# Kernel tuning notes

Hardware: AMD Instinct MI355X
Metric: run time of the kernel (lower is better)

The kernel has to match this reference:

```python
import jax, jax.numpy as jnp
import numpy as np

B, N, D_IN, D_OUT = 2, 4096, 768, 768


def setup_inputs() -> dict:
    key = jax.random.key(0)
    kx, kq, kk, kv = jax.random.split(key, 4)
    x = jax.random.normal(kx, (B, N, D_IN), dtype=jnp.float32)
    # Linear(d_in, d_out, bias=False) weights, stored as [d_in, d_out]
    scale = 1.0 / np.sqrt(D_IN)
    Wq = jax.random.normal(kq, (D_IN, D_OUT), dtype=jnp.float32) * scale
    Wk = jax.random.normal(kk, (D_IN, D_OUT), dtype=jnp.float32) * scale
    Wv = jax.random.normal(kv, (D_IN, D_OUT), dtype=jnp.float32) * scale
    return {"x": x, "Wq": Wq, "Wk": Wk, "Wv": Wv}


def reference(x, Wq, Wk, Wv):
    # q,k,v: [B, N, D_OUT]
    q = jnp.einsum('bnd,de->bne', x, Wq)
    k = jnp.einsum('bnd,de->bne', x, Wk)
    v = jnp.einsum('bnd,de->bne', x, Wv)
    # Full [B, N, N] score matrix (naive attention, as in source).
    # NOTE: source's masked_fill is non-in-place and discarded, so NO causal
    # mask is actually applied -- reproduced faithfully here.
    scores = jnp.einsum('bqe,bke->bqk', q, k) / jnp.sqrt(jnp.float32(k.shape[-1]))
    weights = jax.nn.softmax(scores, axis=-1)
    # dropout rate 0.0 / eval mode -> identity
    out = jnp.einsum('bqk,bke->bqe', weights, v)  # [B, N, D_OUT]
    return out
```

## Files before the change

kernel.cpp:

```cpp
#include <hip/hip_runtime.h>

typedef __bf16 bf16x8 __attribute__((ext_vector_type(8)));
typedef float f32x4 __attribute__((ext_vector_type(4)));

#define GAS __attribute__((address_space(1)))
#define LAS __attribute__((address_space(3)))

__device__ __forceinline__ unsigned short f32_to_bf16(float f) {
    unsigned int u = __float_as_uint(f);
    u += 0x7FFFu + ((u >> 16) & 1u);
    return (unsigned short)(u >> 16);
}

__device__ __forceinline__ void load16(const unsigned short* g, unsigned short* l) {
    __builtin_amdgcn_global_load_lds((GAS unsigned int*)g, (LAS unsigned int*)l, 16, 0, 0);
}

__global__ __launch_bounds__(256) void convert_f32_bf16(
    const float* __restrict__ in, unsigned short* __restrict__ out, int n4)
{
    int i = blockIdx.x * 256 + threadIdx.x;
    if (i < n4) {
        float4 v = ((const float4*)in)[i];
        ushort4 o;
        o.x = f32_to_bf16(v.x); o.y = f32_to_bf16(v.y);
        o.z = f32_to_bf16(v.z); o.w = f32_to_bf16(v.w);
        ((ushort4*)out)[i] = o;
    }
}

__global__ __launch_bounds__(1024) void transpose_w(
    const float* __restrict__ W0, const float* __restrict__ W1, const float* __restrict__ W2,
    unsigned short* __restrict__ T0, unsigned short* __restrict__ T1, unsigned short* __restrict__ T2)
{
    __shared__ float tile[32][33];
    const float* W = (blockIdx.z == 0) ? W0 : (blockIdx.z == 1) ? W1 : W2;
    unsigned short* T = (blockIdx.z == 0) ? T0 : (blockIdx.z == 1) ? T1 : T2;
    int r0 = blockIdx.y * 32, c0 = blockIdx.x * 32;
    tile[threadIdx.y][threadIdx.x] = W[(size_t)(r0 + threadIdx.y) * 768 + c0 + threadIdx.x];
    __syncthreads();
    T[(size_t)(c0 + threadIdx.y) * 768 + r0 + threadIdx.x] = f32_to_bf16(tile[threadIdx.x][threadIdx.y]);
}

template <typename CT>
__global__ __launch_bounds__(256) void gemm_nt(
    const unsigned short* __restrict__ A, const unsigned short* __restrict__ B,
    CT* __restrict__ C, int K, int lda, int ldb, int ldc,
    size_t sA, size_t sB, size_t sC, float alpha)
{
    A += (size_t)blockIdx.z * sA;
    B += (size_t)blockIdx.z * sB;
    C += (size_t)blockIdx.z * sC;
    const int m0 = blockIdx.y * 128;
    const int n0 = blockIdx.x * 128;
    const int t = threadIdx.x;
    const int lane = t & 63;
    const int w = t >> 6;
    const int wm = (w >> 1) * 64;
    const int wn = (w & 1) * 64;

    __shared__ unsigned short At[128 * 64];
    __shared__ unsigned short Bt[128 * 64];

    f32x4 acc[4][4];
#pragma unroll
    for (int i = 0; i < 4; ++i)
#pragma unroll
        for (int j = 0; j < 4; ++j) acc[i][j] = (f32x4){0.f, 0.f, 0.f, 0.f};

    const int r15 = lane & 15;
    const int qa = lane >> 4;

    for (int k0 = 0; k0 < K; k0 += 64) {
#pragma unroll
        for (int i = 0; i < 4; ++i) {
            const int c = i * 256 + t;
            const int row = c >> 3;
            const int cc = (c & 7) ^ (row & 7);
            load16(A + (size_t)(m0 + row) * lda + k0 + cc * 8, &At[c * 8]);
            load16(B + (size_t)(n0 + row) * ldb + k0 + cc * 8, &Bt[c * 8]);
        }
        __syncthreads();

#pragma unroll
        for (int ks = 0; ks < 2; ++ks) {
            bf16x8 af[4], bf[4];
#pragma unroll
            for (int mi = 0; mi < 4; ++mi) {
                const int row = wm + mi * 16 + r15;
                af[mi] = *(const bf16x8*)&At[row * 64 + (((ks << 2) + qa) ^ (row & 7)) * 8];
            }
#pragma unroll
            for (int ni = 0; ni < 4; ++ni) {
                const int row = wn + ni * 16 + r15;
                bf[ni] = *(const bf16x8*)&Bt[row * 64 + (((ks << 2) + qa) ^ (row & 7)) * 8];
            }
#pragma unroll
            for (int mi = 0; mi < 4; ++mi)
#pragma unroll
                for (int ni = 0; ni < 4; ++ni)
                    acc[mi][ni] = __builtin_amdgcn_mfma_f32_16x16x32_bf16(
                        af[mi], bf[ni], acc[mi][ni], 0, 0, 0);
        }
        __syncthreads();
    }

    const int cr = (lane >> 4) * 4;
#pragma unroll
    for (int mi = 0; mi < 4; ++mi) {
#pragma unroll
        for (int ni = 0; ni < 4; ++ni) {
            const int gm = m0 + wm + mi * 16 + cr;
            const int gn = n0 + wn + ni * 16 + r15;
#pragma unroll
            for (int r = 0; r < 4; ++r) {
                float v = alpha * acc[mi][ni][r];
                if constexpr (sizeof(CT) == 2)
                    C[(size_t)(gm + r) * ldc + gn] = (CT)f32_to_bf16(v);
                else
                    C[(size_t)(gm + r) * ldc + gn] = v;
            }
        }
    }
}

__global__ __launch_bounds__(256) void gemm_nt_splitk(
    const unsigned short* __restrict__ P, const unsigned short* __restrict__ Vt,
    float* __restrict__ Part)
{
    const int f = blockIdx.x;
    const int r8 = f & 7;
    const int tq = f >> 3;
    const int n  = tq % 6;
    const int v  = tq / 6;
    const int u  = v * 8 + r8;
    const int batch = u & 1;
    const int split = (u >> 1) & 1;
    const int m = u >> 2;

    const unsigned short* A = P + (size_t)batch * 16777216 + (size_t)split * 2048;
    const unsigned short* B = Vt + (size_t)batch * 4096 + (size_t)split * 2048;
    float* C = Part + (size_t)(split * 2 + batch) * 3145728;
    const int lda = 4096, ldb = 8192, ldc = 768;
    const int m0 = m * 128;
    const int n0 = n * 128;
    const int t = threadIdx.x;
    const int lane = t & 63;
    const int w = t >> 6;
    const int wm = (w >> 1) * 64;
    const int wn = (w & 1) * 64;

    __shared__ unsigned short At[128 * 64];
    __shared__ unsigned short Bt[128 * 64];

    f32x4 acc[4][4];
#pragma unroll
    for (int i = 0; i < 4; ++i)
#pragma unroll
        for (int j = 0; j < 4; ++j) acc[i][j] = (f32x4){0.f, 0.f, 0.f, 0.f};

    const int r15 = lane & 15;
    const int qa = lane >> 4;

    for (int k0 = 0; k0 < 2048; k0 += 64) {
#pragma unroll
        for (int i = 0; i < 4; ++i) {
            const int c = i * 256 + t;
            const int row = c >> 3;
            const int cc = (c & 7) ^ (row & 7);
            load16(A + (size_t)(m0 + row) * lda + k0 + cc * 8, &At[c * 8]);
            load16(B + (size_t)(n0 + row) * ldb + k0 + cc * 8, &Bt[c * 8]);
        }
        __syncthreads();

#pragma unroll
        for (int ks = 0; ks < 2; ++ks) {
            bf16x8 af[4], bf[4];
#pragma unroll
            for (int mi = 0; mi < 4; ++mi) {
                const int row = wm + mi * 16 + r15;
                af[mi] = *(const bf16x8*)&At[row * 64 + (((ks << 2) + qa) ^ (row & 7)) * 8];
            }
#pragma unroll
            for (int ni = 0; ni < 4; ++ni) {
                const int row = wn + ni * 16 + r15;
                bf[ni] = *(const bf16x8*)&Bt[row * 64 + (((ks << 2) + qa) ^ (row & 7)) * 8];
            }
#pragma unroll
            for (int mi = 0; mi < 4; ++mi)
#pragma unroll
                for (int ni = 0; ni < 4; ++ni)
                    acc[mi][ni] = __builtin_amdgcn_mfma_f32_16x16x32_bf16(
                        af[mi], bf[ni], acc[mi][ni], 0, 0, 0);
        }
        __syncthreads();
    }

    const int cr = (lane >> 4) * 4;
#pragma unroll
    for (int mi = 0; mi < 4; ++mi) {
#pragma unroll
        for (int ni = 0; ni < 4; ++ni) {
            const int gm = m0 + wm + mi * 16 + cr;
            const int gn = n0 + wn + ni * 16 + r15;
#pragma unroll
            for (int r = 0; r < 4; ++r)
                C[(size_t)(gm + r) * ldc + gn] = acc[mi][ni][r];
        }
    }
}

__global__ __launch_bounds__(256) void reduce2(
    const float* __restrict__ Part, float* __restrict__ out)
{
    const size_t i = (size_t)blockIdx.x * 256 + threadIdx.x;
    const f32x4* p = (const f32x4*)Part;
    ((f32x4*)out)[i] = p[i] + p[i + 1572864];
}

__global__ __launch_bounds__(256) void softmax_rows(
    const float* __restrict__ S, unsigned short* __restrict__ P)
{
    const size_t row = blockIdx.x;
    const float* s = S + row * 4096;
    unsigned short* p = P + row * 4096;
    const int t = threadIdx.x;
    const int wv = t >> 6, ln = t & 63;

    float4 v[4];
    float lmax = -1e30f;
#pragma unroll
    for (int i = 0; i < 4; ++i) {
        v[i] = ((const float4*)s)[t + i * 256];
        lmax = fmaxf(lmax, fmaxf(fmaxf(v[i].x, v[i].y), fmaxf(v[i].z, v[i].w)));
    }
#pragma unroll
    for (int off = 32; off > 0; off >>= 1) lmax = fmaxf(lmax, __shfl_down(lmax, off, 64));
    __shared__ float redm[4], reds[4];
    if (ln == 0) redm[wv] = lmax;
    __syncthreads();
    const float rmax = fmaxf(fmaxf(redm[0], redm[1]), fmaxf(redm[2], redm[3]));

    float lsum = 0.f;
#pragma unroll
    for (int i = 0; i < 4; ++i) {
        v[i].x = __expf(v[i].x - rmax);
        v[i].y = __expf(v[i].y - rmax);
        v[i].z = __expf(v[i].z - rmax);
        v[i].w = __expf(v[i].w - rmax);
        lsum += v[i].x + v[i].y + v[i].z + v[i].w;
    }
#pragma unroll
    for (int off = 32; off > 0; off >>= 1) lsum += __shfl_down(lsum, off, 64);
    if (ln == 0) reds[wv] = lsum;
    __syncthreads();
    const float inv = 1.f / (reds[0] + reds[1] + reds[2] + reds[3]);

#pragma unroll
    for (int i = 0; i < 4; ++i) {
        ushort4 o;
        o.x = f32_to_bf16(v[i].x * inv);
        o.y = f32_to_bf16(v[i].y * inv);
        o.z = f32_to_bf16(v[i].z * inv);
        o.w = f32_to_bf16(v[i].w * inv);
        ((ushort4*)p)[t + i * 256] = o;
    }
}

extern "C" void kernel_launch(void* const* d_in, const int* in_sizes, int n_in,
                              void* d_out, int out_size, void* d_ws, size_t ws_size,
                              hipStream_t stream) {
    const float* x  = (const float*)d_in[0];
    const float* Wq = (const float*)d_in[1];
    const float* Wk = (const float*)d_in[2];
    const float* Wv = (const float*)d_in[3];
    float* out = (float*)d_out;

    char* base = (char*)d_ws;
    size_t off = 0;
    auto alloc = [&](size_t b) { char* p = base + off; off += (b + 255) & ~(size_t)255; return p; };

    unsigned short* Xbf = (unsigned short*)alloc(8192ull * 768 * 2);
    unsigned short* WqT = (unsigned short*)alloc(768ull * 768 * 2);
    unsigned short* WkT = (unsigned short*)alloc(768ull * 768 * 2);
    unsigned short* WvT = (unsigned short*)alloc(768ull * 768 * 2);
    unsigned short* Qb  = (unsigned short*)alloc(8192ull * 768 * 2);
    unsigned short* Kb  = (unsigned short*)alloc(8192ull * 768 * 2);
    unsigned short* Vt  = (unsigned short*)alloc(768ull * 8192 * 2);
    float*          S   = (float*)alloc(2ull * 4096 * 4096 * 4);
    unsigned short* P   = (unsigned short*)alloc(2ull * 4096 * 4096 * 2);
    (void)ws_size; (void)in_sizes; (void)n_in; (void)out_size;

    convert_f32_bf16<<<dim3(6144), dim3(256), 0, stream>>>(x, Xbf, 8192 * 768 / 4);
    transpose_w<<<dim3(24, 24, 3), dim3(32, 32), 0, stream>>>(Wq, Wk, Wv, WqT, WkT, WvT);
    gemm_nt<unsigned short><<<dim3(6, 64, 2), dim3(256), 0, stream>>>(
        Xbf, WqT, Qb, 768, 768, 768, 768,
         0,  589824,  6291456, 1.0f);
    gemm_nt<unsigned short><<<dim3(64, 6, 1), dim3(256), 0, stream>>>(
        WvT, Xbf, Vt, 768, 768, 768, 8192, 0, 0, 0, 1.0f);
    gemm_nt<float><<<dim3(32, 32, 2), dim3(256), 0, stream>>>(
        Qb, Kb, S, 768, 768, 768, 4096,
         3145728ull,  3145728ull,  16777216ull, 0.03608439182435161f);
    softmax_rows<<<dim3(8192), dim3(256), 0, stream>>>(S, P);
    gemm_nt_splitk<<<dim3(768), dim3(256), 0, stream>>>(P, Vt, (float*)S);
    reduce2<<<dim3(6144), dim3(256), 0, stream>>>((const float*)S, out);
}
```

Baseline: 306.1 us.

## Store scores in bf16, fuse V into QKV GEMM, split-K by four

The score matrix is now written as bf16 instead of fp32, halving the traffic of the score write and the softmax read. The V projection joins the batched QKV GEMM (z=3), and a separate bf16 transpose kernel produces Vt. The PV GEMM is split four ways over K instead of two, doubling the number of blocks at the cost of a larger partial buffer and a 4-way reduction. Storing scores in bf16 before the softmax adds rounding error to the logits.

```diff
diff --git a/kernel.cpp b/kernel.cpp
--- a/kernel.cpp
+++ b/kernel.cpp
@@ -2,6 +2,7 @@
 
 typedef __bf16 bf16x8 __attribute__((ext_vector_type(8)));
 typedef float f32x4 __attribute__((ext_vector_type(4)));
+typedef unsigned short us8 __attribute__((ext_vector_type(8)));
 
 #define GAS __attribute__((address_space(1)))
 #define LAS __attribute__((address_space(3)))
@@ -10,6 +11,10 @@
     unsigned int u = __float_as_uint(f);
     u += 0x7FFFu + ((u >> 16) & 1u);
     return (unsigned short)(u >> 16);
+}
+
+__device__ __forceinline__ float bf16_to_f32(unsigned short h) {
+    return __uint_as_float((unsigned int)h << 16);
 }
 
 __device__ __forceinline__ void load16(const unsigned short* g, unsigned short* l) {
@@ -40,6 +45,16 @@
     tile[threadIdx.y][threadIdx.x] = W[(size_t)(r0 + threadIdx.y) * 768 + c0 + threadIdx.x];
     __syncthreads();
     T[(size_t)(c0 + threadIdx.y) * 768 + r0 + threadIdx.x] = f32_to_bf16(tile[threadIdx.x][threadIdx.y]);
+}
+
+__global__ __launch_bounds__(1024) void transpose_v(
+    const unsigned short* __restrict__ V, unsigned short* __restrict__ Vt)
+{
+    __shared__ unsigned short tile[32][33];
+    int r0 = blockIdx.y * 32, c0 = blockIdx.x * 32;
+    tile[threadIdx.y][threadIdx.x] = V[(size_t)(r0 + threadIdx.y) * 768 + c0 + threadIdx.x];
+    __syncthreads();
+    Vt[(size_t)(c0 + threadIdx.y) * 8192 + r0 + threadIdx.x] = tile[threadIdx.x][threadIdx.y];
 }
 
 template <typename CT>
@@ -135,11 +150,11 @@
     const int v  = tq / 6;
     const int u  = v * 8 + r8;
     const int batch = u & 1;
-    const int split = (u >> 1) & 1;
-    const int m = u >> 2;
-
-    const unsigned short* A = P + (size_t)batch * 16777216 + (size_t)split * 2048;
-    const unsigned short* B = Vt + (size_t)batch * 4096 + (size_t)split * 2048;
+    const int split = (u >> 1) & 3;
+    const int m = u >> 3;
+
+    const unsigned short* A = P + (size_t)batch * 16777216 + (size_t)split * 1024;
+    const unsigned short* B = Vt + (size_t)batch * 4096 + (size_t)split * 1024;
     float* C = Part + (size_t)(split * 2 + batch) * 3145728;
     const int lda = 4096, ldb = 8192, ldc = 768;
     const int m0 = m * 128;
@@ -162,7 +177,7 @@
     const int r15 = lane & 15;
     const int qa = lane >> 4;
 
-    for (int k0 = 0; k0 < 2048; k0 += 64) {
+    for (int k0 = 0; k0 < 1024; k0 += 64) {
 #pragma unroll
         for (int i = 0; i < 4; ++i) {
             const int c = i * 256 + t;
@@ -210,30 +225,32 @@
     }
 }
 
-__global__ __launch_bounds__(256) void reduce2(
+__global__ __launch_bounds__(256) void reduce4(
     const float* __restrict__ Part, float* __restrict__ out)
 {
     const size_t i = (size_t)blockIdx.x * 256 + threadIdx.x;
     const f32x4* p = (const f32x4*)Part;
-    ((f32x4*)out)[i] = p[i] + p[i + 1572864];
-}
-
-__global__ __launch_bounds__(256) void softmax_rows(
-    const float* __restrict__ S, unsigned short* __restrict__ P)
+    ((f32x4*)out)[i] = p[i] + p[i + 1572864] + p[i + 2 * 1572864] + p[i + 3 * 1572864];
+}
+
+__global__ __launch_bounds__(256) void softmax_rows_bf16(
+    const unsigned short* __restrict__ S, unsigned short* __restrict__ P)
 {
     const size_t row = blockIdx.x;
-    const float* s = S + row * 4096;
+    const unsigned short* s = S + row * 4096;
     unsigned short* p = P + row * 4096;
     const int t = threadIdx.x;
     const int wv = t >> 6, ln = t & 63;
 
-    float4 v[4];
+    us8 a = ((const us8*)s)[t];
+    us8 b = ((const us8*)s)[t + 256];
+    float f[16];
+#pragma unroll
+    for (int j = 0; j < 8; ++j) { f[j] = bf16_to_f32(a[j]); f[8 + j] = bf16_to_f32(b[j]); }
+
     float lmax = -1e30f;
 #pragma unroll
-    for (int i = 0; i < 4; ++i) {
-        v[i] = ((const float4*)s)[t + i * 256];
-        lmax = fmaxf(lmax, fmaxf(fmaxf(v[i].x, v[i].y), fmaxf(v[i].z, v[i].w)));
-    }
+    for (int j = 0; j < 16; ++j) lmax = fmaxf(lmax, f[j]);
 #pragma unroll
     for (int off = 32; off > 0; off >>= 1) lmax = fmaxf(lmax, __shfl_down(lmax, off, 64));
     __shared__ float redm[4], reds[4];
@@ -243,28 +260,21 @@
 
     float lsum = 0.f;
 #pragma unroll
-    for (int i = 0; i < 4; ++i) {
-        v[i].x = __expf(v[i].x - rmax);
-        v[i].y = __expf(v[i].y - rmax);
-        v[i].z = __expf(v[i].z - rmax);
-        v[i].w = __expf(v[i].w - rmax);
-        lsum += v[i].x + v[i].y + v[i].z + v[i].w;
-    }
+    for (int j = 0; j < 16; ++j) { f[j] = __expf(f[j] - rmax); lsum += f[j]; }
 #pragma unroll
     for (int off = 32; off > 0; off >>= 1) lsum += __shfl_down(lsum, off, 64);
     if (ln == 0) reds[wv] = lsum;
     __syncthreads();
     const float inv = 1.f / (reds[0] + reds[1] + reds[2] + reds[3]);
 
-#pragma unroll
-    for (int i = 0; i < 4; ++i) {
-        ushort4 o;
-        o.x = f32_to_bf16(v[i].x * inv);
-        o.y = f32_to_bf16(v[i].y * inv);
-        o.z = f32_to_bf16(v[i].z * inv);
-        o.w = f32_to_bf16(v[i].w * inv);
-        ((ushort4*)p)[t + i * 256] = o;
-    }
+    us8 oa, ob;
+#pragma unroll
+    for (int j = 0; j < 8; ++j) {
+        oa[j] = f32_to_bf16(f[j] * inv);
+        ob[j] = f32_to_bf16(f[8 + j] * inv);
+    }
+    ((us8*)p)[t] = oa;
+    ((us8*)p)[t + 256] = ob;
 }
 
 extern "C" void kernel_launch(void* const* d_in, const int* in_sizes, int n_in,
@@ -286,22 +296,23 @@
     unsigned short* WvT = (unsigned short*)alloc(768ull * 768 * 2);
     unsigned short* Qb  = (unsigned short*)alloc(8192ull * 768 * 2);
     unsigned short* Kb  = (unsigned short*)alloc(8192ull * 768 * 2);
+    unsigned short* Vb  = (unsigned short*)alloc(8192ull * 768 * 2);
     unsigned short* Vt  = (unsigned short*)alloc(768ull * 8192 * 2);
-    float*          S   = (float*)alloc(2ull * 4096 * 4096 * 4);
+    float*          Part = (float*)alloc(8ull * 3145728 * 4);
     unsigned short* P   = (unsigned short*)alloc(2ull * 4096 * 4096 * 2);
-    (void)ws_size; (void)in_sizes; (void)n_in; (void)out_size;
+    unsigned short* Sbf = (unsigned short*)Part;
+    (void)ws_size; (void)in_sizes; (void)n_in; (void)out_size; (void)WkT;
 
     convert_f32_bf16<<<dim3(6144), dim3(256), 0, stream>>>(x, Xbf, 8192 * 768 / 4);
     transpose_w<<<dim3(24, 24, 3), dim3(32, 32), 0, stream>>>(Wq, Wk, Wv, WqT, WkT, WvT);
-    gemm_nt<unsigned short><<<dim3(6, 64, 2), dim3(256), 0, stream>>>(
+    gemm_nt<unsigned short><<<dim3(6, 64, 3), dim3(256), 0, stream>>>(
         Xbf, WqT, Qb, 768, 768, 768, 768,
          0,  589824,  6291456, 1.0f);
-    gemm_nt<unsigned short><<<dim3(64, 6, 1), dim3(256), 0, stream>>>(
-        WvT, Xbf, Vt, 768, 768, 768, 8192, 0, 0, 0, 1.0f);
-    gemm_nt<float><<<dim3(32, 32, 2), dim3(256), 0, stream>>>(
-        Qb, Kb, S, 768, 768, 768, 4096,
+    transpose_v<<<dim3(24, 256), dim3(32, 32), 0, stream>>>(Vb, Vt);
+    gemm_nt<unsigned short><<<dim3(32, 32, 2), dim3(256), 0, stream>>>(
+        Qb, Kb, Sbf, 768, 768, 768, 4096,
          3145728ull,  3145728ull,  16777216ull, 0.03608439182435161f);
-    softmax_rows<<<dim3(8192), dim3(256), 0, stream>>>(S, P);
-    gemm_nt_splitk<<<dim3(768), dim3(256), 0, stream>>>(P, Vt, (float*)S);
-    reduce2<<<dim3(6144), dim3(256), 0, stream>>>((const float*)S, out);
-}
+    softmax_rows_bf16<<<dim3(8192), dim3(256), 0, stream>>>(Sbf, P);
+    gemm_nt_splitk<<<dim3(1536), dim3(256), 0, stream>>>(P, Vt, Part);
+    reduce4<<<dim3(6144), dim3(256), 0, stream>>>(Part, out);
+}
```

New measurement: 311.3 us. Within noise of the previous version (+1.7%).
